# Performance work log

Hardware: AMD Instinct MI355X
Metric: run time of the kernel (lower is better)

Reference implementation:

```python
import jax, jax.numpy as jnp
import numpy as np

BETA = 0.25
STRIDE = 64  # LCCombine: ConvTranspose1d with ones kernel, kernel_size == stride


def setup_inputs() -> dict:
    key = jax.random.key(0)
    k0, k1, k2, k3 = jax.random.split(key, 4)
    B, Q, K, N = 2, 64, 512, 1024
    n_classes = 256
    n_wav = N * STRIDE - 1
    quant_pred = jax.random.normal(k0, (B, n_classes, n_wav), dtype=jnp.float32)
    ze = jax.random.normal(k1, (B, Q, N), dtype=jnp.float32)
    emb = jax.random.normal(k2, (K, N), dtype=jnp.float32)
    target_wav = jax.random.randint(k3, (B, 1, n_wav), 0, n_classes)
    return {"quant_pred": quant_pred, "ze": ze, "emb": emb, "target_wav": target_wav}


def _combine(x):
    # LCCombine: replicate each bottleneck-rate value over STRIDE wav steps
    # (transposed conv, ones kernel, kernel==stride), then drop last step.
    # x: (B, N) -> (B, 1, N*STRIDE - 1)
    return jnp.repeat(x, STRIDE, axis=-1)[:, None, :-1]


def reference(quant_pred, ze, emb, target_wav):
    # l2 loss: stop-grad on ze (codebook update term)
    sg_ze = jax.lax.stop_gradient(ze)
    d = sg_ze[:, :, None, :] - emb[None, None, :, :]      # (B, Q, K, N)
    l2_loss = jnp.min(jnp.sum(d * d, axis=1), axis=1)      # (B, N)
    # commitment loss: stop-grad on emb
    sg_emb = jax.lax.stop_gradient(emb)
    dc = ze[:, :, None, :] - sg_emb[None, None, :, :]      # (B, Q, K, N)
    com_loss = jnp.min(jnp.sum(dc * dc, axis=1), axis=1) * BETA  # (B, N)

    l2_loss_comb = _combine(l2_loss)                       # (B, 1, N_wav)
    com_loss_comb = _combine(com_loss)                     # (B, 1, N_wav)

    log_pred = jax.nn.log_softmax(quant_pred, axis=1)      # (B, C, N_wav)
    log_pred_target = jnp.take_along_axis(log_pred, target_wav, axis=1)  # (B,1,N_wav)

    total_loss_terms = log_pred_target + l2_loss_comb + com_loss_comb
    return jnp.mean(total_loss_terms)
```

## Files before the change

### kernel.cpp

```cpp
#include <hip/hip_runtime.h>


#define QQ   64
#define NN   1024
#define KK   512
#define CLS  256
#define NW   65535

__global__ __launch_bounds__(64) void vq_l2min_kernel(
        const float* __restrict__ ze,
        const float* __restrict__ emb,
        float* __restrict__ l2ws,
        float* __restrict__ out) {
    int bn = blockIdx.x;
    int b  = bn >> 10;
    int n  = bn & (NN - 1);
    int lane = threadIdx.x;

    float v  = ze[(size_t)(b * QQ + lane) * NN + n];
    float s1 = v, s2 = v * v;
    #pragma unroll
    for (int m = 32; m >= 1; m >>= 1) {
        s1 += __shfl_xor(s1, m, 64);
        s2 += __shfl_xor(s2, m, 64);
    }

    float best = 3.4e38f;
    float n2s1 = -2.0f * s1;
    #pragma unroll
    for (int j = 0; j < KK / 64; ++j) {
        float e = emb[(size_t)(lane + 64 * j) * NN + n];
        float c = fmaf(e, fmaf((float)QQ, e, n2s1), s2);
        best = fminf(best, c);
    }
    #pragma unroll
    for (int m = 32; m >= 1; m >>= 1)
        best = fminf(best, __shfl_xor(best, m, 64));

    if (lane == 0) l2ws[bn] = 1.25f * best;
    if (bn == 0 && lane == 0) out[0] = 0.0f;
}

__global__ __launch_bounds__(256) void vq_lse_kernel(
        const float* __restrict__ qp,
        const int*   __restrict__ tgt,
        const float* __restrict__ l2ws,
        float* __restrict__ out) {
    int g = blockIdx.x * 256 + threadIdx.x;
    int b = g >> 16;
    int t = g & 0xFFFF;

    float contrib = 0.0f;
    if (t < NW) {
        const float* p = qp + (size_t)b * CLS * NW + t;
        int   tg = tgt[(size_t)b * NW + t];
        float m = -3.4e38f, s = 0.0f, tv = 0.0f;
        #pragma unroll 4
        for (int c = 0; c < CLS; c += 4) {
            float x0 = p[(size_t)(c + 0) * NW];
            float x1 = p[(size_t)(c + 1) * NW];
            float x2 = p[(size_t)(c + 2) * NW];
            float x3 = p[(size_t)(c + 3) * NW];
            if (tg == c + 0) tv = x0;
            if (tg == c + 1) tv = x1;
            if (tg == c + 2) tv = x2;
            if (tg == c + 3) tv = x3;
            float m01 = fmaxf(x0, x1), m23 = fmaxf(x2, x3);
            float m4  = fmaxf(m01, m23);
            float s4  = __expf(x0 - m4) + __expf(x1 - m4)
                      + __expf(x2 - m4) + __expf(x3 - m4);
            float nm  = fmaxf(m, m4);
            s = s * __expf(m - nm) + s4 * __expf(m4 - nm);
            m = nm;
        }
        float lse = m + __logf(s);
        contrib = tv - lse + l2ws[b * NN + (t >> 6)];
    }

    #pragma unroll
    for (int msk = 32; msk >= 1; msk >>= 1)
        contrib += __shfl_xor(contrib, msk, 64);

    __shared__ float part[4];
    int lane = threadIdx.x & 63, wv = threadIdx.x >> 6;
    if (lane == 0) part[wv] = contrib;
    __syncthreads();
    if (threadIdx.x == 0) {
        float blk = part[0] + part[1] + part[2] + part[3];
        atomicAdd(out, blk * (1.0f / 131070.0f));
    }
}

extern "C" void kernel_launch(void* const* d_in, const int* in_sizes, int n_in,
                              void* d_out, int out_size, void* d_ws, size_t ws_size,
                              hipStream_t stream) {
    const float* quant_pred = (const float*)d_in[0];
    const float* ze         = (const float*)d_in[1];
    const float* emb        = (const float*)d_in[2];
    const int*   target     = (const int*)  d_in[3];
    float* out  = (float*)d_out;
    float* l2ws = (float*)d_ws;

    vq_l2min_kernel<<<2 * NN, 64, 0, stream>>>(ze, emb, l2ws, out);
    vq_lse_kernel<<<512, 256, 0, stream>>>(quant_pred, target, l2ws, out);
}
```

Baseline: 202.1 us.

## Split class dimension across waves in LSE kernel and serialize codebook loop per thread

The log-softmax kernel now splits the 256 classes across four waves per block, each handling 64 timesteps, and merges partial max/sum/target values through shared memory. This raises the grid from 512 to 2048 blocks and shortens each thread's serial chain, aiming for more memory parallelism on the bandwidth-bound quant_pred read. The L2-min kernel becomes one thread per (b,n) looping over all Q and K, launched with only 8 blocks. That removes the wave shuffles but leaves little parallelism and long serial loops in that kernel.

```diff
diff --git a/kernel.cpp b/kernel.cpp
--- a/kernel.cpp
+++ b/kernel.cpp
@@ -7,38 +7,34 @@
 #define CLS  256
 #define NW   65535
 
-__global__ __launch_bounds__(64) void vq_l2min_kernel(
+__global__ __launch_bounds__(256) void vq_l2min_kernel(
         const float* __restrict__ ze,
         const float* __restrict__ emb,
         float* __restrict__ l2ws,
         float* __restrict__ out) {
-    int bn = blockIdx.x;
-    int b  = bn >> 10;
-    int n  = bn & (NN - 1);
-    int lane = threadIdx.x;
+    int g = blockIdx.x * 256 + threadIdx.x;
+    int b = g >> 10;
+    int n = g & (NN - 1);
 
-    float v  = ze[(size_t)(b * QQ + lane) * NN + n];
-    float s1 = v, s2 = v * v;
-    #pragma unroll
-    for (int m = 32; m >= 1; m >>= 1) {
-        s1 += __shfl_xor(s1, m, 64);
-        s2 += __shfl_xor(s2, m, 64);
+    float s1 = 0.0f, s2 = 0.0f;
+    #pragma unroll 8
+    for (int q = 0; q < QQ; ++q) {
+        float v = ze[(size_t)(b * QQ + q) * NN + n];
+        s1 += v;
+        s2 = fmaf(v, v, s2);
     }
 
     float best = 3.4e38f;
     float n2s1 = -2.0f * s1;
-    #pragma unroll
-    for (int j = 0; j < KK / 64; ++j) {
-        float e = emb[(size_t)(lane + 64 * j) * NN + n];
+    #pragma unroll 8
+    for (int k = 0; k < KK; ++k) {
+        float e = emb[(size_t)k * NN + n];
         float c = fmaf(e, fmaf((float)QQ, e, n2s1), s2);
         best = fminf(best, c);
     }
-    #pragma unroll
-    for (int m = 32; m >= 1; m >>= 1)
-        best = fminf(best, __shfl_xor(best, m, 64));
 
-    if (lane == 0) l2ws[bn] = 1.25f * best;
-    if (bn == 0 && lane == 0) out[0] = 0.0f;
+    l2ws[g] = 1.25f * best;
+    if (g == 0) out[0] = 0.0f;
 }
 
 __global__ __launch_bounds__(256) void vq_lse_kernel(
@@ -46,48 +42,61 @@
         const int*   __restrict__ tgt,
         const float* __restrict__ l2ws,
         float* __restrict__ out) {
-    int g = blockIdx.x * 256 + threadIdx.x;
-    int b = g >> 16;
-    int t = g & 0xFFFF;
+    int blk  = blockIdx.x;
+    int b    = blk >> 10;
+    int tc   = blk & 1023;
+    int lane = threadIdx.x & 63;
+    int wv   = threadIdx.x >> 6;
 
-    float contrib = 0.0f;
-    if (t < NW) {
-        const float* p = qp + (size_t)b * CLS * NW + t;
-        int   tg = tgt[(size_t)b * NW + t];
-        float m = -3.4e38f, s = 0.0f, tv = 0.0f;
-        #pragma unroll 4
-        for (int c = 0; c < CLS; c += 4) {
-            float x0 = p[(size_t)(c + 0) * NW];
-            float x1 = p[(size_t)(c + 1) * NW];
-            float x2 = p[(size_t)(c + 2) * NW];
-            float x3 = p[(size_t)(c + 3) * NW];
-            if (tg == c + 0) tv = x0;
-            if (tg == c + 1) tv = x1;
-            if (tg == c + 2) tv = x2;
-            if (tg == c + 3) tv = x3;
-            float m01 = fmaxf(x0, x1), m23 = fmaxf(x2, x3);
-            float m4  = fmaxf(m01, m23);
-            float s4  = __expf(x0 - m4) + __expf(x1 - m4)
-                      + __expf(x2 - m4) + __expf(x3 - m4);
-            float nm  = fmaxf(m, m4);
-            s = s * __expf(m - nm) + s4 * __expf(m4 - nm);
-            m = nm;
-        }
-        float lse = m + __logf(s);
-        contrib = tv - lse + l2ws[b * NN + (t >> 6)];
+    int t  = tc * 64 + lane;
+    int tl = t < NW ? t : NW - 1;
+
+    const float* p = qp + (size_t)b * CLS * NW + (size_t)(wv * 64) * NW + tl;
+    int tg = tgt[(size_t)b * NW + tl] - wv * 64;
+
+    float m = -3.4e38f, s = 0.0f, tv = 0.0f;
+    #pragma unroll 4
+    for (int c = 0; c < 64; c += 4) {
+        float x0 = p[(size_t)(c + 0) * NW];
+        float x1 = p[(size_t)(c + 1) * NW];
+        float x2 = p[(size_t)(c + 2) * NW];
+        float x3 = p[(size_t)(c + 3) * NW];
+        if (tg == c + 0) tv = x0;
+        if (tg == c + 1) tv = x1;
+        if (tg == c + 2) tv = x2;
+        if (tg == c + 3) tv = x3;
+        float m01 = fmaxf(x0, x1), m23 = fmaxf(x2, x3);
+        float m4  = fmaxf(m01, m23);
+        float s4  = __expf(x0 - m4) + __expf(x1 - m4)
+                  + __expf(x2 - m4) + __expf(x3 - m4);
+        float nm  = fmaxf(m, m4);
+        s = s * __expf(m - nm) + s4 * __expf(m4 - nm);
+        m = nm;
     }
 
-    #pragma unroll
-    for (int msk = 32; msk >= 1; msk >>= 1)
-        contrib += __shfl_xor(contrib, msk, 64);
+    __shared__ float sm[4][64], ss[4][64], st[4][64];
+    sm[wv][lane] = m;
+    ss[wv][lane] = s;
+    st[wv][lane] = tv;
+    __syncthreads();
 
-    __shared__ float part[4];
-    int lane = threadIdx.x & 63, wv = threadIdx.x >> 6;
-    if (lane == 0) part[wv] = contrib;
-    __syncthreads();
-    if (threadIdx.x == 0) {
-        float blk = part[0] + part[1] + part[2] + part[3];
-        atomicAdd(out, blk * (1.0f / 131070.0f));
+    if (wv == 0) {
+        float m0 = sm[0][lane], m1 = sm[1][lane],
+              m2 = sm[2][lane], m3 = sm[3][lane];
+        float M  = fmaxf(fmaxf(m0, m1), fmaxf(m2, m3));
+        float S  = ss[0][lane] * __expf(m0 - M) + ss[1][lane] * __expf(m1 - M)
+                 + ss[2][lane] * __expf(m2 - M) + ss[3][lane] * __expf(m3 - M);
+        float TV = st[0][lane] + st[1][lane] + st[2][lane] + st[3][lane];
+        float lse = M + __logf(S);
+
+        float l2 = l2ws[b * NN + tc];
+        float contrib = (t < NW) ? (TV - lse + l2) : 0.0f;
+
+        #pragma unroll
+        for (int msk = 32; msk >= 1; msk >>= 1)
+            contrib += __shfl_xor(contrib, msk, 64);
+        if (lane == 0)
+            atomicAdd(out, contrib * (1.0f / 131070.0f));
     }
 }
 
@@ -101,6 +110,6 @@
     float* out  = (float*)d_out;
     float* l2ws = (float*)d_ws;
 
-    vq_l2min_kernel<<<2 * NN, 64, 0, stream>>>(ze, emb, l2ws, out);
-    vq_lse_kernel<<<512, 256, 0, stream>>>(quant_pred, target, l2ws, out);
+    vq_l2min_kernel<<<8, 256, 0, stream>>>(ze, emb, l2ws, out);
+    vq_lse_kernel<<<2 * NN, 256, 0, stream>>>(quant_pred, target, l2ws, out);
 }
```

After: 327.6 us. 1.62x slower.
